# Kernel tuning notes

Hardware: AMD Instinct MI355X
Metric: run time of the kernel (lower is better)

The kernel has to match this reference:

```python
import jax, jax.numpy as jnp
import numpy as np

K = 10000  # number of distinct duration values (duration value == segment id)


def setup_inputs() -> dict:
    key = jax.random.key(0)
    k1, k2, k3 = jax.random.split(key, 3)
    N = 8_000_000
    log_h = jax.random.normal(k1, (N,), dtype=jnp.float32)
    durations = jax.random.randint(k2, (N,), 0, K, dtype=jnp.int32)
    events = jax.random.randint(k3, (N,), 0, 2, dtype=jnp.int32)
    return {"log_h": log_h, "durations": durations, "events": events}


def _cox_ph_loss(log_h, durations, events):
    e = events.astype(jnp.float32)
    # cox_ph_loss: permute events/log_h by DESCENDING duration (durations stay original)
    idx_desc = jnp.argsort(-durations)
    e2 = e[idx_desc]
    lh2 = log_h[idx_desc]
    # cox_ph_loss_sorted: ascending sort of the ORIGINAL durations
    idx_asc = jnp.argsort(durations)
    sorted_dur = durations[idx_asc]          # ascending durations
    sorted_events = e2[idx_asc]              # desc-permuted events re-gathered (faithful)
    pred_surv = jnp.exp(lh2)                 # hazards (grad flows here)
    # baseline(): groupby duration of {expg=exp(log_h.detach()), event},
    # cumsum over DESCENDING durations, hazard = event_sum / risk_set_sum
    expg = jnp.exp(jax.lax.stop_gradient(lh2))
    expg_sum = jax.ops.segment_sum(expg, durations, num_segments=K)   # [K]
    ev_sum = jax.ops.segment_sum(e2, durations, num_segments=K)       # [K]
    risk = jnp.cumsum(expg_sum[::-1])[::-1]   # sum of expg over durations >= t
    base = jnp.where(risk > 0.0, ev_sum / risk, 0.0)                  # [K]
    # repeated_base loop == gather baseline hazard at each sample's duration
    repeated_base = base[sorted_dur]
    pred = repeated_base * pred_surv
    mse = jnp.mean((pred - sorted_events) ** 2)
    # CoxPHLoss.forward: zero loss if no events
    return jnp.where(jnp.sum(e) == 0, jnp.float32(0.0), mse)


def reference(log_h, durations, events):
    return _cox_ph_loss(log_h, durations, events)
```

## Files before the change

kernel.cpp:

```cpp
#include <hip/hip_runtime.h>

#define KSEG 10000
#define NBLK 256
#define HALF 5000
#define RECMAX 17000
#define GBIN 8
#define CAPE 8192

typedef unsigned long long u64;
typedef unsigned int u32;
typedef unsigned short u16;
typedef unsigned char u8;

__global__ __launch_bounds__(1024) void localsort_lds(const int* __restrict__ dur,
                                                      const float* __restrict__ log_h,
                                                      const int* __restrict__ events,
                                                      u64* __restrict__ S,
                                                      u16* __restrict__ Pb,
                                                      int N, int chunk) {
    __shared__ u64 rec[RECMAX];
    __shared__ u32 cp[KSEG / 2];
    __shared__ u32 wsum[16];
    __shared__ u32 carry_s, pb_half;
    u32* h32 = (u32*)rec;

    int b = blockIdx.x;
    int s = b * chunk, e = min(N, s + chunk);
    int tid = threadIdx.x;
    int lane = tid & 63, wid = tid >> 6;
    int kiter = (chunk + 1023) >> 10;

    for (int i = tid; i < KSEG; i += 1024) h32[i] = 0;
    if (tid == 0) carry_s = 0;
    __syncthreads();

    int myd[32];
    for (int k = 0; k < kiter; ++k) {
        int j = s + tid + (k << 10);
        int d = -1;
        if (j < e) { d = dur[j]; atomicAdd(&h32[d], 1); }
        myd[k] = d;
    }
    __syncthreads();

    for (int base = 0; base < KSEG; base += 1024) {
        int t = base + tid;
        u32 h = (t < KSEG) ? h32[t] : 0;
        u32 v = h;
        for (int off = 1; off < 64; off <<= 1) {
            u32 x = __shfl_up(v, off);
            if (lane >= off) v += x;
        }
        if (lane == 63) wsum[wid] = v;
        __syncthreads();
        if (wid == 0) {
            u32 wv = (lane < 16) ? wsum[lane] : 0;
            for (int off = 1; off < 16; off <<= 1) {
                u32 x = __shfl_up(wv, off);
                if (lane >= off) wv += x;
            }
            if (lane < 16) wsum[lane] = wv;
        }
        __syncthreads();
        u32 incl = v + ((wid > 0) ? wsum[wid - 1] : 0) + carry_s;
        u32 excl = incl - h;
        if (t < KSEG) {
            Pb[(size_t)b * (KSEG + 1) + t] = (u16)excl;
            if (!(t & 1)) cp[t >> 1] = excl | (incl << 16);
            if (t == HALF) pb_half = excl;
        }
        __syncthreads();
        if (tid == 1023) carry_s = incl;
    }
    __syncthreads();
    u32 total = carry_s;
    if (tid == 0) Pb[(size_t)b * (KSEG + 1) + KSEG] = (u16)total;
    u32 base0 = pb_half;
    __syncthreads();

    for (int ph = 0; ph < 2; ++ph) {
        int t0 = ph ? HALF : 0;
        u32 pbase = ph ? base0 : 0;
        u32 plen = ph ? (total - base0) : base0;
        for (int k = 0; k < kiter; ++k) {
            int d = myd[k];
            if ((unsigned)(d - t0) < (unsigned)HALF) {
                int j = s + tid + (k << 10);
                u32 add = (d & 1) ? 0x10000u : 1u;
                u32 old = atomicAdd(&cp[d >> 1], add);
                u32 pos = (d & 1) ? (old >> 16) : (old & 0xffffu);
                u32 hi = ((u32)j << 1) | (u32)events[j];
                rec[pos - pbase] = ((u64)hi << 32) | (u64)__float_as_uint(log_h[j]);
            }
        }
        __syncthreads();
        for (u32 i = tid; i < plen; i += 1024) S[(size_t)s + pbase + i] = rec[i];
        __syncthreads();
    }
}

__global__ void colscan_counts(const u16* __restrict__ Pb, int* __restrict__ counts) {
    int t = blockIdx.x * blockDim.x + threadIdx.x;
    if (t >= KSEG) return;
    int run = 0;
    for (int b = 0; b < NBLK; ++b) {
        const u16* row = Pb + (size_t)b * (KSEG + 1);
        run += (int)row[t + 1] - (int)row[t];
    }
    counts[t] = run;
}

__global__ void scan_kernel(const int* __restrict__ counts, int* __restrict__ cum, int K) {
    __shared__ int sm[1024];
    __shared__ int carry_s;
    int tid = threadIdx.x;
    if (tid == 0) carry_s = 0;
    __syncthreads();
    for (int base = 0; base < K; base += 1024) {
        int v = (base + tid < K) ? counts[base + tid] : 0;
        sm[tid] = v;
        __syncthreads();
        for (int off = 1; off < 1024; off <<= 1) {
            int t = (tid >= off) ? sm[tid - off] : 0;
            __syncthreads();
            sm[tid] += t;
            __syncthreads();
        }
        int carry = carry_s;
        if (base + tid < K) cum[base + tid] = carry + sm[tid] - v;
        __syncthreads();
        if (tid == 1023) carry_s = carry + sm[1023];
        __syncthreads();
    }
    if (tid == 0) cum[K] = carry_s;
}

__global__ void transpose_pb(const u16* __restrict__ Pb, u16* __restrict__ PbT) {
    __shared__ u16 tile[64][65];
    int t0 = blockIdx.x * 64;
    int b0 = blockIdx.y * 64;
    int tx = threadIdx.x;
    int ty = threadIdx.y;
    for (int r = ty; r < 64; r += 4) {
        int b = b0 + r, t = t0 + tx;
        tile[r][tx] = (b < NBLK && t <= KSEG) ? Pb[(size_t)b * (KSEG + 1) + t] : (u16)0;
    }
    __syncthreads();
    for (int r = ty; r < 64; r += 4) {
        int t = t0 + r, b = b0 + tx;
        if (t <= KSEG && b < NBLK) PbT[(size_t)t * NBLK + b] = tile[tx][r];
    }
}

__global__ __launch_bounds__(512) void runsort_pe4(const u64* __restrict__ S,
                                                   const int* __restrict__ cum,
                                                   const u16* __restrict__ PbT,
                                                   float* __restrict__ P,
                                                   u32* __restrict__ J,
                                                   u32* __restrict__ E2w,
                                                   u16* __restrict__ binhint,
                                                   int N, int chunk) {
    __shared__ u64 sm[CAPE];
    __shared__ int L[GBIN * 256];
    __shared__ u16 rows[(GBIN + 1) * 256];
    __shared__ int t512[512];
    __shared__ int cumLoc[GBIN + 1];
    __shared__ u32 bits[128];
    __shared__ u32 wpart[8];

    int t0 = blockIdx.x * GBIN;
    int G2 = min(GBIN, KSEG - t0);
    if (G2 <= 0) return;
    int tid = threadIdx.x;
    int lane = tid & 63, wid = tid >> 6;

    for (int i = tid; i < (G2 + 1) * 256; i += 512) {
        int t = i >> 8, b = i & 255;
        rows[i] = PbT[(size_t)(t0 + t) * NBLK + b];
    }
    if (tid <= G2) cumLoc[tid] = cum[t0 + tid];
    __syncthreads();

    int u = 0;
    while (u < G2) {
        int m = 1;
        while (u + m < G2 && cumLoc[u + m + 1] - cumLoc[u] <= CAPE) ++m;
        int aBatch = cumLoc[u];

        for (int i = tid; i < GBIN * 256; i += 512) {
            int tt = i >> 8, b = i & 255;
            int v = 0;
            if (tt < m)
                v = (int)rows[(u + tt + 1) * 256 + b] - (int)rows[(u + tt) * 256 + b];
            L[i] = v;
        }
        __syncthreads();

        int r4[4];
        int base4 = tid * 4, sum4 = 0;
        for (int k = 0; k < 4; ++k) { r4[k] = sum4; sum4 += L[base4 + k]; }
        t512[tid] = sum4;
        __syncthreads();
        {
            int v = t512[tid];
            for (int off = 1; off < 64; off <<= 1) {
                int x = __shfl_up(v, off);
                if (lane >= off) v += x;
            }
            if (lane == 63) wpart[wid] = (u32)v;
            __syncthreads();
            if (tid == 0) {
                u32 run = 0;
                for (int w = 0; w < 8; ++w) { u32 tmp = wpart[w]; wpart[w] = run; run += tmp; }
            }
            __syncthreads();
            int excl = v - sum4 + (int)wpart[wid];
            for (int k = 0; k < 4; ++k) r4[k] += excl;
        }
        __syncthreads();
        for (int k = 0; k < 4; ++k) L[base4 + k] = r4[k];
        __syncthreads();

        for (int i = tid; i < m * 256; i += 512) {
            int tt = i >> 8, b = i & 255;
            int r0 = (int)rows[(u + tt) * 256 + b];
            int l = (int)rows[(u + tt + 1) * 256 + b] - r0;
            int o = L[i];
            const u64* src = S + (size_t)b * chunk + r0;
            for (int k = 0; k < l; ++k) sm[o + k] = src[k];
            for (int k = 1; k < l; ++k) {
                u64 key = sm[o + k];
                int jj = o + k - 1;
                while (jj >= o && sm[jj] > key) { sm[jj + 1] = sm[jj]; --jj; }
                sm[jj + 1] = key;
            }
        }
        __syncthreads();

        for (int tt = 0; tt < m; ++tt) {
            int t = u + tt;
            int a = cumLoc[t], b = cumLoc[t + 1];
            int c = b - a;
            int lbase = a - aBatch;
            int q0 = N - b;
            int nw = (c + 31) >> 5;
            for (int k = tid; k < nw; k += 512) bits[k] = 0;
            __syncthreads();
            for (int i = tid; i < c; i += 512) {
                u64 rec = sm[lbase + i];
                P[q0 + i] = expf(__uint_as_float((u32)rec));
                J[a + i] = (u32)(rec >> 33);
                if (rec & 0x100000000ull) atomicOr(&bits[i >> 5], 1u << (i & 31));
            }
            __syncthreads();
            for (int k = tid; k < nw; k += 512) {
                u32 v = bits[k];
                if (!v) continue;
                long gb = (long)q0 + 32l * k;
                int w = (int)(gb >> 5), sh = (int)(gb & 31);
                atomicOr(&E2w[w], v << sh);
                if (sh && (v >> (32 - sh))) atomicOr(&E2w[w + 1], v >> (32 - sh));
            }
            if (tid == 0) {
                for (int k = (a + 255) >> 8; (k << 8) < b; ++k) binhint[k] = (u16)(t0 + t);
            }
            __syncthreads();
        }
        u += m;
    }
}

__global__ __launch_bounds__(1024) void sums3(const int* __restrict__ dur,
                                              const float* __restrict__ P,
                                              const u32* __restrict__ E2w,
                                              float* __restrict__ expg_part,
                                              u16* __restrict__ evs_part,
                                              int N, int chunk) {
    __shared__ float he[KSEG];
    __shared__ int hv[KSEG];
    for (int i = threadIdx.x; i < KSEG; i += blockDim.x) { he[i] = 0.f; hv[i] = 0; }
    __syncthreads();
    int b = blockIdx.x;
    int s = b * chunk, e = min(N, s + chunk);
    for (int j = s + threadIdx.x; j < e; j += blockDim.x) {
        int t = dur[j];
        atomicAdd(&he[t], P[j]);
        if ((E2w[j >> 5] >> (j & 31)) & 1u) atomicAdd(&hv[t], 1);
    }
    __syncthreads();
    for (int i = threadIdx.x; i < KSEG; i += blockDim.x) {
        expg_part[(size_t)b * KSEG + i] = he[i];
        evs_part[(size_t)b * KSEG + i] = (u16)hv[i];
    }
}

__global__ void reduce_sums(const float* __restrict__ expg_part,
                            const u16* __restrict__ evs_part,
                            float* __restrict__ expg, float* __restrict__ evs, int B) {
    int t = blockIdx.x * blockDim.x + threadIdx.x;
    if (t >= KSEG) return;
    float a = 0.f;
    int v = 0;
    for (int b = 0; b < B; ++b) {
        a += expg_part[(size_t)b * KSEG + t];
        v += (int)evs_part[(size_t)b * KSEG + t];
    }
    expg[t] = a;
    evs[t] = (float)v;
}

__global__ void baseline_kernel(const float* __restrict__ expg, const float* __restrict__ evs,
                                float* __restrict__ base, float* __restrict__ ev_total, int K) {
    __shared__ float sm[1024];
    __shared__ float carry_s;
    int tid = threadIdx.x;
    if (tid == 0) carry_s = 0.f;
    float evloc = 0.f;
    __syncthreads();
    for (int b = 0; b < K; b += 1024) {
        int u = b + tid;
        int t = K - 1 - u;
        float v = 0.f, ev = 0.f;
        if (u < K) { v = expg[t]; ev = evs[t]; }
        evloc += ev;
        sm[tid] = v;
        __syncthreads();
        for (int off = 1; off < 1024; off <<= 1) {
            float x = (tid >= off) ? sm[tid - off] : 0.f;
            __syncthreads();
            sm[tid] += x;
            __syncthreads();
        }
        float carry = carry_s;
        if (u < K) {
            float risk = carry + sm[tid];
            base[t] = (risk > 0.f) ? ev / risk : 0.f;
        }
        __syncthreads();
        if (tid == 1023) carry_s = carry + sm[1023];
        __syncthreads();
    }
    sm[tid] = evloc;
    __syncthreads();
    for (int o = 512; o > 0; o >>= 1) {
        if (tid < o) sm[tid] += sm[tid + o];
        __syncthreads();
    }
    if (tid == 0) ev_total[0] = sm[0];
}

__global__ __launch_bounds__(1024) void mse4(const float* __restrict__ P,
                                             const u32* __restrict__ J,
                                             const u32* __restrict__ E2w,
                                             const int* __restrict__ cum,
                                             const u16* __restrict__ binhint,
                                             const float* __restrict__ base,
                                             double* __restrict__ acc, int N) {
    int stride = gridDim.x * blockDim.x;
    double s = 0.0;
    for (int i = blockIdx.x * blockDim.x + threadIdx.x; i < N; i += stride) {
        int t = (int)binhint[i >> 8];
        while (cum[t + 1] <= i) ++t;
        u32 x = J[i];
        float ev = (float)((E2w[x >> 5] >> (x & 31)) & 1u);
        float d = base[t] * P[i] - ev;
        s += (double)d * (double)d;
    }
    __shared__ double sm[1024];
    sm[threadIdx.x] = s;
    __syncthreads();
    for (int o = 512; o > 0; o >>= 1) {
        if ((int)threadIdx.x < o) sm[threadIdx.x] += sm[threadIdx.x + o];
        __syncthreads();
    }
    if (threadIdx.x == 0) atomicAdd(acc, sm[0]);
}

__global__ void final_kernel(const double* __restrict__ acc, const float* __restrict__ ev_total,
                             float* __restrict__ out, int N) {
    out[0] = (ev_total[0] == 0.f) ? 0.0f : (float)(*acc / (double)N);
}

extern "C" void kernel_launch(void* const* d_in, const int* in_sizes, int n_in,
                              void* d_out, int out_size, void* d_ws, size_t ws_size,
                              hipStream_t stream) {
    const float* log_h = (const float*)d_in[0];
    const int* dur     = (const int*)d_in[1];
    const int* events  = (const int*)d_in[2];
    int N = in_sizes[0];
    float* out = (float*)d_out;

    char* ws = (char*)d_ws;
    size_t off = 0;
    auto alloc = [&](size_t bytes) -> char* {
        char* p = ws + off;
        off = (off + bytes + 255) & ~(size_t)255;
        return p;
    };
    double* acc  = (double*)alloc(8);
    u32*    E2w  = (u32*)alloc(((size_t)N / 32 + 2) * 4);
    size_t zero_bytes = off;
    float*  ev_total = (float*)alloc(4);
    int*    counts   = (int*)alloc(KSEG * 4);
    int*    cum      = (int*)alloc((KSEG + 1) * 4);
    float*  expg     = (float*)alloc(KSEG * 4);
    float*  evs      = (float*)alloc(KSEG * 4);
    float*  base     = (float*)alloc(KSEG * 4);
    u16*    binhint  = (u16*)alloc(((size_t)N / 256 + 1) * 2);
    u16*    Pb       = (u16*)alloc((size_t)NBLK * (KSEG + 1) * 2);
    u16*    PbT      = (u16*)alloc((size_t)(KSEG + 1) * NBLK * 2);
    u64*    S        = (u64*)alloc((size_t)N * 8);
    float*  P        = (float*)alloc((size_t)N * 4);
    u32*    J        = (u32*)alloc((size_t)N * 4);
    (void)ws_size;

    float* expg_part = (float*)S;
    u16*   evs_part  = (u16*)((char*)S + (size_t)NBLK * KSEG * 4 + 256);

    int chunk = (N + NBLK - 1) / NBLK;

    hipMemsetAsync(d_ws, 0, zero_bytes, stream);

    localsort_lds<<<NBLK, 1024, 0, stream>>>(dur, log_h, events, S, Pb, N, chunk);
    colscan_counts<<<(KSEG + 255) / 256, 256, 0, stream>>>(Pb, counts);
    scan_kernel<<<1, 1024, 0, stream>>>(counts, cum, KSEG);
    transpose_pb<<<dim3((KSEG + 64) / 64, NBLK / 64), dim3(64, 4), 0, stream>>>(Pb, PbT);
    runsort_pe4<<<(KSEG + GBIN - 1) / GBIN, 512, 0, stream>>>(S, cum, PbT, P, J, E2w,
                                                              binhint, N, chunk);
    sums3<<<NBLK, 1024, 0, stream>>>(dur, P, E2w, expg_part, evs_part, N, chunk);
    reduce_sums<<<(KSEG + 255) / 256, 256, 0, stream>>>(expg_part, evs_part, expg, evs, NBLK);
    baseline_kernel<<<1, 1024, 0, stream>>>(expg, evs, base, ev_total, KSEG);
    mse4<<<512, 1024, 0, stream>>>(P, J, E2w, cum, binhint, base, acc, N);
    final_kernel<<<1, 1, 0, stream>>>(acc, ev_total, out, N);
}
```

Baseline: 494.2 us.

## Cache log_h and events in registers during local sort; halve run-sort batch size

```diff
diff --git a/kernel.cpp b/kernel.cpp
--- a/kernel.cpp
+++ b/kernel.cpp
@@ -4,15 +4,16 @@
 #define NBLK 256
 #define HALF 5000
 #define RECMAX 17000
-#define GBIN 8
-#define CAPE 8192
+#define KITER 31
+#define GBIN 4
+#define CAPE 4096
 
 typedef unsigned long long u64;
 typedef unsigned int u32;
 typedef unsigned short u16;
 typedef unsigned char u8;
 
-__global__ __launch_bounds__(1024) void localsort_lds(const int* __restrict__ dur,
+__global__ __launch_bounds__(1024) void localsort_reg(const int* __restrict__ dur,
                                                       const float* __restrict__ log_h,
                                                       const int* __restrict__ events,
                                                       u64* __restrict__ S,
@@ -28,19 +29,29 @@
     int s = b * chunk, e = min(N, s + chunk);
     int tid = threadIdx.x;
     int lane = tid & 63, wid = tid >> 6;
-    int kiter = (chunk + 1023) >> 10;
 
     for (int i = tid; i < KSEG; i += 1024) h32[i] = 0;
     if (tid == 0) carry_s = 0;
     __syncthreads();
 
-    int myd[32];
-    for (int k = 0; k < kiter; ++k) {
+    u32 md[KITER];
+    float mlh[KITER];
+#pragma unroll
+    for (int k = 0; k < KITER; ++k) {
         int j = s + tid + (k << 10);
-        int d = -1;
-        if (j < e) { d = dur[j]; atomicAdd(&h32[d], 1); }
-        myd[k] = d;
-    }
+        u32 pack = 0xFFFFu;
+        float lh = 0.f;
+        if (j < e) {
+            int d = dur[j];
+            pack = (u32)d | ((u32)(events[j] != 0) << 14);
+            lh = log_h[j];
+            atomicAdd(&h32[d], 1);
+        }
+        md[k] = pack;
+        mlh[k] = lh;
+    }
+    for (int j = s + tid + (KITER << 10); j < e; j += 1024)
+        atomicAdd(&h32[dur[j]], 1);
     __syncthreads();
 
     for (int base = 0; base < KSEG; base += 1024) {
@@ -82,14 +93,26 @@
         int t0 = ph ? HALF : 0;
         u32 pbase = ph ? base0 : 0;
         u32 plen = ph ? (total - base0) : base0;
-        for (int k = 0; k < kiter; ++k) {
-            int d = myd[k];
+#pragma unroll
+        for (int k = 0; k < KITER; ++k) {
+            int d = (int)(md[k] & 0x3FFFu);
             if ((unsigned)(d - t0) < (unsigned)HALF) {
                 int j = s + tid + (k << 10);
+                u32 ev = (md[k] >> 14) & 1u;
                 u32 add = (d & 1) ? 0x10000u : 1u;
                 u32 old = atomicAdd(&cp[d >> 1], add);
                 u32 pos = (d & 1) ? (old >> 16) : (old & 0xffffu);
-                u32 hi = ((u32)j << 1) | (u32)events[j];
+                u32 hi = ((u32)j << 1) | ev;
+                rec[pos - pbase] = ((u64)hi << 32) | (u64)__float_as_uint(mlh[k]);
+            }
+        }
+        for (int j = s + tid + (KITER << 10); j < e; j += 1024) {
+            int d = dur[j];
+            if ((unsigned)(d - t0) < (unsigned)HALF) {
+                u32 add = (d & 1) ? 0x10000u : 1u;
+                u32 old = atomicAdd(&cp[d >> 1], add);
+                u32 pos = (d & 1) ? (old >> 16) : (old & 0xffffu);
+                u32 hi = ((u32)j << 1) | (u32)(events[j] != 0);
                 rec[pos - pbase] = ((u64)hi << 32) | (u64)__float_as_uint(log_h[j]);
             }
         }
@@ -196,10 +219,10 @@
         }
         __syncthreads();
 
-        int r4[4];
-        int base4 = tid * 4, sum4 = 0;
-        for (int k = 0; k < 4; ++k) { r4[k] = sum4; sum4 += L[base4 + k]; }
-        t512[tid] = sum4;
+        int r2[2];
+        int base2 = tid * 2, sum2 = 0;
+        for (int k = 0; k < 2; ++k) { r2[k] = sum2; sum2 += L[base2 + k]; }
+        t512[tid] = sum2;
         __syncthreads();
         {
             int v = t512[tid];
@@ -214,11 +237,11 @@
                 for (int w = 0; w < 8; ++w) { u32 tmp = wpart[w]; wpart[w] = run; run += tmp; }
             }
             __syncthreads();
-            int excl = v - sum4 + (int)wpart[wid];
-            for (int k = 0; k < 4; ++k) r4[k] += excl;
-        }
-        __syncthreads();
-        for (int k = 0; k < 4; ++k) L[base4 + k] = r4[k];
+            int excl = v - sum2 + (int)wpart[wid];
+            for (int k = 0; k < 2; ++k) r2[k] += excl;
+        }
+        __syncthreads();
+        for (int k = 0; k < 2; ++k) L[base2 + k] = r2[k];
         __syncthreads();
 
         for (int i = tid; i < m * 256; i += 512) {
@@ -421,7 +444,7 @@
 
     hipMemsetAsync(d_ws, 0, zero_bytes, stream);
 
-    localsort_lds<<<NBLK, 1024, 0, stream>>>(dur, log_h, events, S, Pb, N, chunk);
+    localsort_reg<<<NBLK, 1024, 0, stream>>>(dur, log_h, events, S, Pb, N, chunk);
     colscan_counts<<<(KSEG + 255) / 256, 256, 0, stream>>>(Pb, counts);
     scan_kernel<<<1, 1024, 0, stream>>>(counts, cum, KSEG);
     transpose_pb<<<dim3((KSEG + 64) / 64, NBLK / 64), dim3(64, 4), 0, stream>>>(Pb, PbT);
```

Result: slower. 505.5 us (+2.3%).
